# Performance work log

Hardware: AMD Instinct MI355X
Metric: run time of the kernel (lower is better)

## Reference

```python
import jax, jax.numpy as jnp
import numpy as np

EPS = 1e-9


def setup_inputs() -> dict:
    key = jax.random.key(0)
    k1, k2 = jax.random.split(key)
    B, IN, OUT = 16384, 2048, 2048
    x = jax.random.normal(k1, (B, IN), dtype=jnp.float32)
    w = jax.random.normal(k2, (OUT, IN), dtype=jnp.float32)
    # set_weight_norms_to(initial_weight_norm=0.01): rescale each row's L2 norm to 0.01
    wn = jnp.linalg.norm(w, axis=1, keepdims=True)
    weight = 0.01 * w / (wn + 1e-10)
    logprior = jnp.zeros((OUT,), dtype=jnp.float32)
    lamb = jnp.float32(4.0)  # initial_lambda
    return {"x": x, "weight": weight, "logprior": logprior, "lamb": lamb}


def reference(x, weight, logprior, lamb):
    # L2-normalize inputs per row
    x_n = x / (jnp.linalg.norm(x, axis=1, keepdims=True) + EPS)  # [B, IN]
    # L2-normalize weight rows -> cosine similarities
    W = weight / (jnp.linalg.norm(weight, axis=1, keepdims=True) + EPS)  # [OUT, IN]
    a = x_n @ W.T  # [B, OUT] cosine sims
    # RePU inhibition, triangle=False -> setpoint 0
    u = jax.nn.relu(a)
    un = u / (jnp.max(u) + EPS)  # global max normalization
    # power-law with logprior; safe power (0**lamb == 0) to keep grads clean
    pos = un > 0
    ulamb = jnp.where(pos, jnp.where(pos, un, 1.0) ** lamb, 0.0) * jnp.exp(logprior)
    y = ulamb / (jnp.sum(ulamb, axis=1, keepdims=True) + EPS)
    return y
```

## Files before the change

### kernel.cpp

```cpp
#include <hip/hip_runtime.h>
#include <hip/hip_bf16.h>

typedef unsigned short u16;
typedef __attribute__((ext_vector_type(8))) short bf16x8;
typedef __attribute__((ext_vector_type(4))) float f32x4;

#define EPSN 1e-9f


__device__ __forceinline__ u16 f2bf(float f) {
    union { float f; unsigned int u; } c; c.f = f;
    unsigned int u = c.u;
    unsigned int r = (u + 0x7FFFu + ((u >> 16) & 1u)) >> 16;
    return (u16)r;
}

__device__ __forceinline__ void load16_to_lds(const void* g, void* l) {
    __builtin_amdgcn_global_load_lds(
        (const __attribute__((address_space(1))) void*)g,
        (__attribute__((address_space(3))) void*)l,
        16, 0, 0);
}

__global__ __launch_bounds__(256) void normalize_cast(
    const float* __restrict__ X, u16* __restrict__ Y, int ncols) {
    const size_t row = blockIdx.x;
    const float4* xr = (const float4*)(X + row * (size_t)ncols);
    const int nq = ncols >> 2;

    float ss = 0.f;
    for (int i = threadIdx.x; i < nq; i += 256) {
        float4 v = xr[i];
        ss += v.x*v.x + v.y*v.y + v.z*v.z + v.w*v.w;
    }
    #pragma unroll
    for (int o = 32; o > 0; o >>= 1) ss += __shfl_down(ss, o);

    __shared__ float red[4];
    __shared__ float scale_sh;
    const int lane = threadIdx.x & 63, wv = threadIdx.x >> 6;
    if (lane == 0) red[wv] = ss;
    __syncthreads();
    if (threadIdx.x == 0) {
        float t = red[0] + red[1] + red[2] + red[3];
        scale_sh = 1.f / (sqrtf(t) + EPSN);
    }
    __syncthreads();
    const float s = scale_sh;

    ushort4* yr = (ushort4*)(Y + row * (size_t)ncols);
    for (int i = threadIdx.x; i < nq; i += 256) {
        float4 v = xr[i];
        ushort4 o4;
        o4.x = f2bf(v.x * s); o4.y = f2bf(v.y * s);
        o4.z = f2bf(v.z * s); o4.w = f2bf(v.w * s);
        yr[i] = o4;
    }
}

__global__ void prep_explp(const float* __restrict__ lp, float* __restrict__ out, int n) {
    int i = blockIdx.x * blockDim.x + threadIdx.x;
    if (i < n) out[i] = expf(lp[i]);
}

#define BK 64

__global__ __launch_bounds__(256, 1) void gemm_softhebb(
    const u16* __restrict__ A, const u16* __restrict__ B,
    const float* __restrict__ explp, const float* __restrict__ lambp,
    float* __restrict__ Ul, float* __restrict__ rowsum,
    int M, int N, int K) {
    __shared__ __align__(16) u16 lA[128 * BK];
    __shared__ __align__(16) u16 lB[128 * BK];

    const int tid  = threadIdx.x;
    const int lane = tid & 63;
    const int wm   = (tid >> 6) & 1;
    const int wn   = tid >> 7;
    const int row0 = blockIdx.y * 128;
    const int col0 = blockIdx.x * 128;

    const u16* Ag = A + (size_t)row0 * K;
    const u16* Bg = B + (size_t)col0 * K;

    f32x4 acc[4][4] = {};

    int srow[4], soff[4];
    #pragma unroll
    for (int p = 0; p < 4; ++p) {
        int c = p * 256 + tid;
        int r = c >> 3;
        srow[p] = r;
        soff[p] = ((c & 7) ^ (r & 7)) * 8;
    }

    for (int k0 = 0; k0 < K; k0 += BK) {
        #pragma unroll
        for (int p = 0; p < 4; ++p) {
            int c = p * 256 + tid;
            load16_to_lds(Ag + (size_t)srow[p] * K + k0 + soff[p], &lA[c * 8]);
            load16_to_lds(Bg + (size_t)srow[p] * K + k0 + soff[p], &lB[c * 8]);
        }
        __syncthreads();

        #pragma unroll
        for (int s = 0; s < 2; ++s) {
            const int pos = (((s << 2) + (lane >> 4)) ^ (lane & 7)) * 8;
            bf16x8 af[4], bfr[4];
            #pragma unroll
            for (int i = 0; i < 4; ++i) {
                int r = wm * 64 + i * 16 + (lane & 15);
                af[i] = *(const bf16x8*)&lA[r * 64 + pos];
            }
            #pragma unroll
            for (int j = 0; j < 4; ++j) {
                int r = wn * 64 + j * 16 + (lane & 15);
                bfr[j] = *(const bf16x8*)&lB[r * 64 + pos];
            }
            #pragma unroll
            for (int i = 0; i < 4; ++i)
                #pragma unroll
                for (int j = 0; j < 4; ++j)
                    acc[i][j] = __builtin_amdgcn_mfma_f32_16x16x32_bf16(
                        af[i], bfr[j], acc[i][j], 0, 0, 0);
        }
        __syncthreads();
    }

    const float lam = *lambp;
    const bool lam4 = (lam == 4.0f);
    #pragma unroll
    for (int i = 0; i < 4; ++i) {
        #pragma unroll
        for (int p = 0; p < 4; ++p) {
            const int m = row0 + wm * 64 + i * 16 + (lane >> 4) * 4 + p;
            float rs = 0.f;
            #pragma unroll
            for (int j = 0; j < 4; ++j) {
                const int n = col0 + wn * 64 + j * 16 + (lane & 15);
                float a = acc[i][j][p];
                float u = 0.f;
                if (a > 0.f) {
                    float pw;
                    if (lam4) { float a2 = a * a; pw = a2 * a2; }
                    else      { pw = __powf(a, lam); }
                    u = pw * explp[n];
                }
                Ul[(size_t)m * N + n] = u;
                rs += u;
            }
            rs += __shfl_xor(rs, 1);
            rs += __shfl_xor(rs, 2);
            rs += __shfl_xor(rs, 4);
            rs += __shfl_xor(rs, 8);
            if ((lane & 15) == 0) atomicAdd(&rowsum[m], rs);
        }
    }
}

__global__ __launch_bounds__(256) void finalize_div(
    float* __restrict__ Ul, const float* __restrict__ rowsum,
    int nq_per_row, long total_q) {
    long i = (long)blockIdx.x * blockDim.x + threadIdx.x;
    const long stride = (long)gridDim.x * blockDim.x;
    for (; i < total_q; i += stride) {
        int row = (int)(i / nq_per_row);
        float inv = 1.f / (rowsum[row] + EPSN);
        float4 v = ((const float4*)Ul)[i];
        v.x *= inv; v.y *= inv; v.z *= inv; v.w *= inv;
        ((float4*)Ul)[i] = v;
    }
}

static inline size_t align256(size_t x) { return (x + 255) & ~(size_t)255; }

extern "C" void kernel_launch(void* const* d_in, const int* in_sizes, int n_in,
                              void* d_out, int out_size, void* d_ws, size_t ws_size,
                              hipStream_t stream) {
    const float* x        = (const float*)d_in[0];
    const float* w        = (const float*)d_in[1];
    const float* logprior = (const float*)d_in[2];
    const float* lamb     = (const float*)d_in[3];
    const int OUT = in_sizes[2];
    const int IN  = in_sizes[1] / OUT;
    const int B   = in_sizes[0] / IN;
    float* out = (float*)d_out;

    char* ws = (char*)d_ws;
    size_t off = 0;
    u16* xn = (u16*)(ws + off);        off += align256((size_t)B * IN * sizeof(u16));
    u16* wn = (u16*)(ws + off);        off += align256((size_t)OUT * IN * sizeof(u16));
    float* rowsum = (float*)(ws + off); off += align256((size_t)B * sizeof(float));
    float* explp  = (float*)(ws + off); off += align256((size_t)OUT * sizeof(float));

    hipMemsetAsync(rowsum, 0, (size_t)B * sizeof(float), stream);
    normalize_cast<<<B, 256, 0, stream>>>(x, xn, IN);
    normalize_cast<<<OUT, 256, 0, stream>>>(w, wn, IN);
    prep_explp<<<(OUT + 255) / 256, 256, 0, stream>>>(logprior, explp, OUT);

    dim3 grid(OUT / 128, B / 128);
    gemm_softhebb<<<grid, 256, 0, stream>>>(xn, wn, explp, lamb, out, rowsum, B, OUT, IN);

    long total_q = (long)B * OUT / 4;
    finalize_div<<<8192, 256, 0, stream>>>(out, rowsum, OUT / 4, total_q);
}
```

Measured before the change: 500.0 us.

## Cache row in registers for normalize, precompute GEMM pointers, per-row finalize

```diff
diff --git a/kernel.cpp b/kernel.cpp
--- a/kernel.cpp
+++ b/kernel.cpp
@@ -22,16 +22,22 @@
         16, 0, 0);
 }
 
+#define MAXQ 8
 __global__ __launch_bounds__(256) void normalize_cast(
     const float* __restrict__ X, u16* __restrict__ Y, int ncols) {
     const size_t row = blockIdx.x;
     const float4* xr = (const float4*)(X + row * (size_t)ncols);
     const int nq = ncols >> 2;
 
+    float4 v[MAXQ];
     float ss = 0.f;
-    for (int i = threadIdx.x; i < nq; i += 256) {
-        float4 v = xr[i];
-        ss += v.x*v.x + v.y*v.y + v.z*v.z + v.w*v.w;
+    #pragma unroll
+    for (int k = 0; k < MAXQ; ++k) {
+        int i = threadIdx.x + k * 256;
+        if (i < nq) {
+            v[k] = xr[i];
+            ss += v[k].x*v[k].x + v[k].y*v[k].y + v[k].z*v[k].z + v[k].w*v[k].w;
+        }
     }
     #pragma unroll
     for (int o = 32; o > 0; o >>= 1) ss += __shfl_down(ss, o);
@@ -49,12 +55,15 @@
     const float s = scale_sh;
 
     ushort4* yr = (ushort4*)(Y + row * (size_t)ncols);
-    for (int i = threadIdx.x; i < nq; i += 256) {
-        float4 v = xr[i];
-        ushort4 o4;
-        o4.x = f2bf(v.x * s); o4.y = f2bf(v.y * s);
-        o4.z = f2bf(v.z * s); o4.w = f2bf(v.w * s);
-        yr[i] = o4;
+    #pragma unroll
+    for (int k = 0; k < MAXQ; ++k) {
+        int i = threadIdx.x + k * 256;
+        if (i < nq) {
+            ushort4 o4;
+            o4.x = f2bf(v[k].x * s); o4.y = f2bf(v[k].y * s);
+            o4.z = f2bf(v[k].z * s); o4.w = f2bf(v[k].w * s);
+            yr[i] = o4;
+        }
     }
 }
 
@@ -65,7 +74,7 @@
 
 #define BK 64
 
-__global__ __launch_bounds__(256, 1) void gemm_softhebb(
+__global__ __launch_bounds__(256, 2) void gemm_softhebb(
     const u16* __restrict__ A, const u16* __restrict__ B,
     const float* __restrict__ explp, const float* __restrict__ lambp,
     float* __restrict__ Ul, float* __restrict__ rowsum,
@@ -80,26 +89,25 @@
     const int row0 = blockIdx.y * 128;
     const int col0 = blockIdx.x * 128;
 
-    const u16* Ag = A + (size_t)row0 * K;
-    const u16* Bg = B + (size_t)col0 * K;
-
     f32x4 acc[4][4] = {};
 
-    int srow[4], soff[4];
+    const u16* ap[4];
+    const u16* bp[4];
     #pragma unroll
     for (int p = 0; p < 4; ++p) {
         int c = p * 256 + tid;
         int r = c >> 3;
-        srow[p] = r;
-        soff[p] = ((c & 7) ^ (r & 7)) * 8;
+        int o = ((c & 7) ^ (r & 7)) * 8;
+        ap[p] = A + (size_t)(row0 + r) * K + o;
+        bp[p] = B + (size_t)(col0 + r) * K + o;
     }
 
     for (int k0 = 0; k0 < K; k0 += BK) {
         #pragma unroll
         for (int p = 0; p < 4; ++p) {
             int c = p * 256 + tid;
-            load16_to_lds(Ag + (size_t)srow[p] * K + k0 + soff[p], &lA[c * 8]);
-            load16_to_lds(Bg + (size_t)srow[p] * K + k0 + soff[p], &lB[c * 8]);
+            load16_to_lds(ap[p] + k0, &lA[c * 8]);
+            load16_to_lds(bp[p] + k0, &lB[c * 8]);
         }
         __syncthreads();
 
@@ -129,24 +137,29 @@
 
     const float lam = *lambp;
     const bool lam4 = (lam == 4.0f);
+    float el[4];
+    #pragma unroll
+    for (int j = 0; j < 4; ++j)
+        el[j] = explp[col0 + wn * 64 + j * 16 + (lane & 15)];
+
     #pragma unroll
     for (int i = 0; i < 4; ++i) {
         #pragma unroll
         for (int p = 0; p < 4; ++p) {
             const int m = row0 + wm * 64 + i * 16 + (lane >> 4) * 4 + p;
+            float* outrow = Ul + (size_t)m * N + col0 + wn * 64 + (lane & 15);
             float rs = 0.f;
             #pragma unroll
             for (int j = 0; j < 4; ++j) {
-                const int n = col0 + wn * 64 + j * 16 + (lane & 15);
                 float a = acc[i][j][p];
                 float u = 0.f;
                 if (a > 0.f) {
                     float pw;
                     if (lam4) { float a2 = a * a; pw = a2 * a2; }
                     else      { pw = __powf(a, lam); }
-                    u = pw * explp[n];
+                    u = pw * el[j];
                 }
-                Ul[(size_t)m * N + n] = u;
+                outrow[j * 16] = u;
                 rs += u;
             }
             rs += __shfl_xor(rs, 1);
@@ -158,17 +171,15 @@
     }
 }
 
-__global__ __launch_bounds__(256) void finalize_div(
-    float* __restrict__ Ul, const float* __restrict__ rowsum,
-    int nq_per_row, long total_q) {
-    long i = (long)blockIdx.x * blockDim.x + threadIdx.x;
-    const long stride = (long)gridDim.x * blockDim.x;
-    for (; i < total_q; i += stride) {
-        int row = (int)(i / nq_per_row);
-        float inv = 1.f / (rowsum[row] + EPSN);
-        float4 v = ((const float4*)Ul)[i];
+__global__ __launch_bounds__(256) void finalize_row(
+    float* __restrict__ Ul, const float* __restrict__ rowsum, int nq) {
+    const size_t row = blockIdx.x;
+    const float inv = 1.f / (rowsum[row] + EPSN);
+    float4* p = (float4*)(Ul + row * (size_t)nq * 4);
+    for (int i = threadIdx.x; i < nq; i += 256) {
+        float4 v = p[i];
         v.x *= inv; v.y *= inv; v.z *= inv; v.w *= inv;
-        ((float4*)Ul)[i] = v;
+        p[i] = v;
     }
 }
 
@@ -201,6 +212,5 @@
     dim3 grid(OUT / 128, B / 128);
     gemm_softhebb<<<grid, 256, 0, stream>>>(xn, wn, explp, lamb, out, rowsum, B, OUT, IN);
 
-    long total_q = (long)B * OUT / 4;
-    finalize_div<<<8192, 256, 0, stream>>>(out, rowsum, OUT / 4, total_q);
-}
+    finalize_row<<<B, 256, 0, stream>>>(out, rowsum, OUT / 4);
+}
```

Result: faster. 414.5 us (-17.1%).
